# Kernel tuning notes

Hardware: AMD Instinct MI355X
Metric: run time of the kernel (lower is better)

Reference implementation:

```python
import jax, jax.numpy as jnp
import numpy as np

EMBED = 1024
HEADS = 16
HEAD_DIM = EMBED // HEADS


def setup_inputs() -> dict:
    key = jax.random.key(0)
    ks = jax.random.split(key, 10)
    N, S, D = 2, 2048, EMBED
    scale = 1.0 / np.sqrt(D)
    inp = {
        "x": jax.random.normal(ks[0], (N, S, D), dtype=jnp.float32),
        "mask": jax.random.randint(ks[1], (N, 1, S, S), 0, 2, dtype=jnp.int32),
        "Wq": jax.random.normal(ks[2], (D, D), dtype=jnp.float32) * scale,
        "bq": jnp.zeros((D,), dtype=jnp.float32),
        "Wk": jax.random.normal(ks[3], (D, D), dtype=jnp.float32) * scale,
        "bk": jnp.zeros((D,), dtype=jnp.float32),
        "Wv": jax.random.normal(ks[4], (D, D), dtype=jnp.float32) * scale,
        "bv": jnp.zeros((D,), dtype=jnp.float32),
        "Wo": jax.random.normal(ks[5], (D, D), dtype=jnp.float32) * scale,
        "bo": jnp.zeros((D,), dtype=jnp.float32),
    }
    return inp


def reference(x, mask, Wq, bq, Wk, bk, Wv, bv, Wo, bo):
    N, S, D = x.shape
    H, Hd = HEADS, HEAD_DIM
    def split_heads(t):
        return t.reshape(N, S, H, Hd).transpose(0, 2, 1, 3)  # [N,H,S,Hd]
    q = split_heads(x @ Wq + bq)
    k = split_heads(x @ Wk + bk)
    v = split_heads(x @ Wv + bv)
    scores = jnp.einsum("nhqd,nhkd->nhqk", q, k) / jnp.sqrt(jnp.float32(Hd))
    scores = jnp.where(mask == 0, jnp.float32(-jnp.inf), scores)
    attn = jax.nn.softmax(scores, axis=-1)
    out = jnp.einsum("nhqk,nhkd->nhqd", attn, v)
    out = out.transpose(0, 2, 1, 3).reshape(N, S, D)
    return out @ Wo + bo
```

## Files before the change

### kernel.cpp

```cpp
#include <hip/hip_runtime.h>
#include <stdint.h>


typedef _Float16 h8 __attribute__((ext_vector_type(8)));
typedef _Float16 h4 __attribute__((ext_vector_type(4)));
typedef float f32x4 __attribute__((ext_vector_type(4)));

#define MFMA16(a, b, c) __builtin_amdgcn_mfma_f32_16x16x32_f16(a, b, c, 0, 0, 0)

static __device__ __forceinline__ int swz128(int row, int colB) {
    return (row * 128 + colB) ^ ((row & 7) << 4);
}

__global__ __launch_bounds__(256) void k_pack_mask(const int* __restrict__ mask,
                                                   uint32_t* __restrict__ mp) {
    int i = blockIdx.x * 256 + threadIdx.x;
    unsigned long long b = __ballot(mask[i] != 0);
    if ((threadIdx.x & 63) == 0) {
        *(unsigned long long*)(mp + (i >> 5)) = b;
    }
}

__global__ __launch_bounds__(256) void k_wt(const float* __restrict__ W0,
                                            const float* __restrict__ W1,
                                            const float* __restrict__ W2,
                                            _Float16* __restrict__ out) {
    const int nb = blockIdx.x, kb = blockIdx.y, z = blockIdx.z;
    const float* W = (z == 0) ? W0 : ((z == 1) ? W1 : W2);
    _Float16* O = out + (size_t)z * 1024 * 1024;
    __shared__ __align__(16) _Float16 lds[64][68];
    const int t = threadIdx.x;
    const int k0 = kb * 64, n0 = nb * 64;
#pragma unroll
    for (int p = 0; p < 4; ++p) {
        int idx = t + p * 256;
        int kr = idx >> 4;
        int c = idx & 15;
        float4 v = *(const float4*)(W + (size_t)(k0 + kr) * 1024 + n0 + c * 4);
        h4 hv;
        hv[0] = (_Float16)v.x; hv[1] = (_Float16)v.y;
        hv[2] = (_Float16)v.z; hv[3] = (_Float16)v.w;
        *(h4*)(&lds[kr][c * 4]) = hv;
    }
    __syncthreads();
#pragma unroll
    for (int p = 0; p < 2; ++p) {
        int idx = t + p * 256;
        int n = idx >> 3;
        int kc = idx & 7;
        h8 o;
#pragma unroll
        for (int i = 0; i < 8; ++i) o[i] = lds[kc * 8 + i][n];
        *(h8*)(O + (size_t)(n0 + n) * 1024 + k0 + kc * 8) = o;
    }
}

__global__ __launch_bounds__(256) void k_qkv(const float* __restrict__ X,
                                             const _Float16* __restrict__ Wt,
                                             const float* __restrict__ bq,
                                             const float* __restrict__ bk,
                                             const float* __restrict__ bv,
                                             _Float16* __restrict__ Qo,
                                             _Float16* __restrict__ Ko,
                                             _Float16* __restrict__ VtO) {
    const int nt = blockIdx.x;
    const int mt = blockIdx.y;
    const int z = blockIdx.z;
    const _Float16* W = Wt + (size_t)z * 1024 * 1024;
    const float* bias = (z == 0) ? bq : ((z == 1) ? bk : bv);

    __shared__ __align__(16) char lds[32768];
    char* As = lds;
    char* Bs = lds + 16384;

    const int t = threadIdx.x;
    const int lane = t & 63;
    const int w = t >> 6;
    const int wm = w >> 1, wn = w & 1;
    const int m0 = mt * 128, n0 = nt * 128;

    f32x4 acc[4][4] = {};

    for (int kt = 0; kt < 16; ++kt) {
        const int k0 = kt * 64;
#pragma unroll
        for (int p = 0; p < 8; ++p) {
            int idx = t + p * 256;
            int row = idx >> 4;
            int c4 = idx & 15;
            float4 v = *(const float4*)(X + (size_t)(m0 + row) * 1024 + k0 + c4 * 4);
            h4 hv;
            hv[0] = (_Float16)v.x; hv[1] = (_Float16)v.y;
            hv[2] = (_Float16)v.z; hv[3] = (_Float16)v.w;
            *(h4*)(As + swz128(row, c4 * 8)) = hv;
        }
#pragma unroll
        for (int p = 0; p < 4; ++p) {
            int idx = t + p * 256;
            int row = idx >> 3;
            int c = idx & 7;
            uint4 v = *(const uint4*)(W + (size_t)(n0 + row) * 1024 + k0 + c * 8);
            *(uint4*)(Bs + swz128(row, c * 16)) = v;
        }
        __syncthreads();

#pragma unroll
        for (int kk = 0; kk < 2; ++kk) {
            h8 af[4], bf[4];
#pragma unroll
            for (int fm = 0; fm < 4; ++fm)
                af[fm] = *(h8*)(As + swz128(wm * 64 + fm * 16 + (lane & 15),
                                            kk * 64 + (lane >> 4) * 16));
#pragma unroll
            for (int fn = 0; fn < 4; ++fn)
                bf[fn] = *(h8*)(Bs + swz128(wn * 64 + fn * 16 + (lane & 15),
                                            kk * 64 + (lane >> 4) * 16));
#pragma unroll
            for (int fm = 0; fm < 4; ++fm)
#pragma unroll
                for (int fn = 0; fn < 4; ++fn)
                    acc[fm][fn] = MFMA16(af[fm], bf[fn], acc[fm][fn]);
        }
        __syncthreads();
    }

    if (z == 2) {
#pragma unroll
        for (int fn = 0; fn < 4; ++fn) {
            int n = n0 + wn * 64 + fn * 16 + (lane & 15);
            float bv_ = bias[n];
            int h = n >> 6, d = n & 63;
#pragma unroll
            for (int fm = 0; fm < 4; ++fm) {
                int m_base = m0 + wm * 64 + fm * 16 + (lane >> 4) * 4;
                int bi = m_base >> 11, s0 = m_base & 2047;
                h4 pv;
#pragma unroll
                for (int r = 0; r < 4; ++r) pv[r] = (_Float16)(acc[fm][fn][r] + bv_);
                *(h4*)(VtO + ((size_t)((bi * 16 + h) * 64 + d)) * 2048 + s0) = pv;
            }
        }
    } else {
        _Float16* Out = (z == 0) ? Qo : Ko;
#pragma unroll
        for (int fn = 0; fn < 4; ++fn) {
            int n = n0 + wn * 64 + fn * 16 + (lane & 15);
            float bv_ = bias[n];
            int h = n >> 6, d = n & 63;
#pragma unroll
            for (int fm = 0; fm < 4; ++fm) {
#pragma unroll
                for (int r = 0; r < 4; ++r) {
                    int m = m0 + wm * 64 + fm * 16 + (lane >> 4) * 4 + r;
                    int bi = m >> 11, s = m & 2047;
                    float val = acc[fm][fn][r] + bv_;
                    Out[(size_t)((bi * 16 + h) * 2048 + s) * 64 + d] = (_Float16)val;
                }
            }
        }
    }
}

__global__ __launch_bounds__(256) void k_attn(const _Float16* __restrict__ Q,
                                              const _Float16* __restrict__ K,
                                              const _Float16* __restrict__ Vt,
                                              const uint32_t* __restrict__ mp,
                                              _Float16* __restrict__ ctx) {
    const int qt = blockIdx.x;
    const int nh = blockIdx.y;
    const int bi = nh >> 4;
    const int t = threadIdx.x, lane = t & 63, w = t >> 6;
    const int g = lane >> 4;
    const int q15 = lane & 15;

    __shared__ __align__(16) char lds[24576];
    char* Ks = lds;
    char* Vs = lds + 8192;
    char* Ps = lds + 16384 + w * 2048;

    const int qbase = qt * 64 + w * 16;

    h8 qf[2];
#pragma unroll
    for (int kk = 0; kk < 2; ++kk)
        qf[kk] = *(const h8*)(Q + ((size_t)nh * 2048 + qbase + q15) * 64 + kk * 32 + g * 8);

    f32x4 of[4] = {};
    float lacc = 0.f;

    const size_t kbase = (size_t)nh * 2048 * 64;
    const size_t vbase = (size_t)nh * 64 * 2048;
    const float C1 = 0.18033688f;
    const float C2 = 11.541560f;

    for (int kt = 0; kt < 32; ++kt) {
#pragma unroll
        for (int p = 0; p < 2; ++p) {
            int c = t + p * 256;
            int row = c >> 3;
            int cb = (c & 7) * 16;
            uint4 kv = *(const uint4*)(K + kbase + (size_t)kt * 4096 + c * 8);
            *(uint4*)(Ks + swz128(row, cb)) = kv;
            uint4 vv = *(const uint4*)(Vt + vbase + (size_t)row * 2048 + kt * 64 + (c & 7) * 8);
            *(uint4*)(Vs + swz128(row, cb)) = vv;
        }
        __syncthreads();

        f32x4 sf[4];
#pragma unroll
        for (int fn = 0; fn < 4; ++fn) {
            f32x4 a = {};
#pragma unroll
            for (int kk = 0; kk < 2; ++kk) {
                h8 kf = *(h8*)(Ks + swz128(fn * 16 + q15, kk * 64 + g * 16));
                a = MFMA16(kf, qf[kk], a);
            }
            sf[fn] = a;
        }

        {
            uint2 mw = *(const uint2*)(mp + ((size_t)bi * 2048 + qbase + q15) * 64 + kt * 2);
#pragma unroll
            for (int fn = 0; fn < 4; ++fn) {
                uint32_t word = (fn & 2) ? mw.y : mw.x;
                int bitbase = ((fn & 1) << 4) + g * 4;
                h4 pv4;
#pragma unroll
                for (int r = 0; r < 4; ++r) {
                    float p = ((word >> (bitbase + r)) & 1u)
                                  ? __builtin_amdgcn_exp2f(fmaf(sf[fn][r], C1, -C2))
                                  : 0.f;
                    lacc += p;
                    pv4[r] = (_Float16)p;
                }
                *(h4*)(Ps + swz128(q15, (fn * 16 + g * 4) * 2)) = pv4;
            }
        }

        h8 pa[2];
#pragma unroll
        for (int kk = 0; kk < 2; ++kk)
            pa[kk] = *(h8*)(Ps + swz128(q15, kk * 64 + g * 16));
#pragma unroll
        for (int fn = 0; fn < 4; ++fn) {
#pragma unroll
            for (int kk = 0; kk < 2; ++kk) {
                h8 vb = *(h8*)(Vs + swz128(fn * 16 + q15, kk * 64 + g * 16));
                of[fn] = MFMA16(pa[kk], vb, of[fn]);
            }
        }
        __syncthreads();
    }

    lacc += __shfl_xor(lacc, 16);
    lacc += __shfl_xor(lacc, 32);

#pragma unroll
    for (int r = 0; r < 4; ++r) {
        float lq = __shfl(lacc, g * 4 + r);
        int srow = qbase + g * 4 + r;
#pragma unroll
        for (int fn = 0; fn < 4; ++fn) {
            float val = of[fn][r] / lq;
            ctx[(size_t)(bi * 2048 + srow) * 1024 + (nh & 15) * 64 + fn * 16 + q15] =
                (_Float16)val;
        }
    }
}

__global__ __launch_bounds__(256) void k_oproj(const _Float16* __restrict__ A,
                                               const _Float16* __restrict__ Wot,
                                               const float* __restrict__ bias,
                                               float* __restrict__ out) {
    const int nt = blockIdx.x, mt = blockIdx.y;
    __shared__ __align__(16) char lds[32768];
    char* As = lds;
    char* Bs = lds + 16384;
    const int t = threadIdx.x, lane = t & 63, w = t >> 6;
    const int wm = w >> 1, wn = w & 1;
    const int m0 = mt * 128, n0 = nt * 128;
    f32x4 acc[4][4] = {};

    for (int kt = 0; kt < 16; ++kt) {
        const int k0 = kt * 64;
#pragma unroll
        for (int p = 0; p < 4; ++p) {
            int idx = t + p * 256;
            int row = idx >> 3;
            int c = idx & 7;
            uint4 v = *(const uint4*)(A + (size_t)(m0 + row) * 1024 + k0 + c * 8);
            *(uint4*)(As + swz128(row, c * 16)) = v;
        }
#pragma unroll
        for (int p = 0; p < 4; ++p) {
            int idx = t + p * 256;
            int row = idx >> 3;
            int c = idx & 7;
            uint4 v = *(const uint4*)(Wot + (size_t)(n0 + row) * 1024 + k0 + c * 8);
            *(uint4*)(Bs + swz128(row, c * 16)) = v;
        }
        __syncthreads();

#pragma unroll
        for (int kk = 0; kk < 2; ++kk) {
            h8 af[4], bf[4];
#pragma unroll
            for (int fm = 0; fm < 4; ++fm)
                af[fm] = *(h8*)(As + swz128(wm * 64 + fm * 16 + (lane & 15),
                                            kk * 64 + (lane >> 4) * 16));
#pragma unroll
            for (int fn = 0; fn < 4; ++fn)
                bf[fn] = *(h8*)(Bs + swz128(wn * 64 + fn * 16 + (lane & 15),
                                            kk * 64 + (lane >> 4) * 16));
#pragma unroll
            for (int fm = 0; fm < 4; ++fm)
#pragma unroll
                for (int fn = 0; fn < 4; ++fn)
                    acc[fm][fn] = MFMA16(af[fm], bf[fn], acc[fm][fn]);
        }
        __syncthreads();
    }

#pragma unroll
    for (int fn = 0; fn < 4; ++fn) {
        int n = n0 + wn * 64 + fn * 16 + (lane & 15);
        float b = bias[n];
#pragma unroll
        for (int fm = 0; fm < 4; ++fm) {
#pragma unroll
            for (int r = 0; r < 4; ++r) {
                int m = m0 + wm * 64 + fm * 16 + (lane >> 4) * 4 + r;
                out[(size_t)m * 1024 + n] = acc[fm][fn][r] + b;
            }
        }
    }
}

extern "C" void kernel_launch(void* const* d_in, const int* in_sizes, int n_in,
                              void* d_out, int out_size, void* d_ws, size_t ws_size,
                              hipStream_t stream) {
    const float* x = (const float*)d_in[0];
    const int* mask = (const int*)d_in[1];
    const float* Wq = (const float*)d_in[2];
    const float* bq = (const float*)d_in[3];
    const float* Wk = (const float*)d_in[4];
    const float* bk = (const float*)d_in[5];
    const float* Wv = (const float*)d_in[6];
    const float* bv = (const float*)d_in[7];
    const float* Wo = (const float*)d_in[8];
    const float* bo = (const float*)d_in[9];
    float* out = (float*)d_out;

    char* ws = (char*)d_ws;
    _Float16* Wt = (_Float16*)(ws);
    _Float16* ctx = (_Float16*)(ws);
    _Float16* Q = (_Float16*)(ws + (8u << 20));
    _Float16* Kb = (_Float16*)(ws + (16u << 20));
    _Float16* Vt = (_Float16*)(ws + (24u << 20));
    _Float16* Wot = (_Float16*)(ws + (24u << 20));
    uint32_t* mp = (uint32_t*)(ws + (32u << 20));

    k_pack_mask<<<(2 * 2048 * 2048) / 256, 256, 0, stream>>>(mask, mp);
    k_wt<<<dim3(16, 16, 3), 256, 0, stream>>>(Wq, Wk, Wv, Wt);
    k_qkv<<<dim3(8, 32, 3), 256, 0, stream>>>(x, Wt, bq, bk, bv, Q, Kb, Vt);
    k_attn<<<dim3(32, 32), 256, 0, stream>>>(Q, Kb, Vt, mp, ctx);
    k_wt<<<dim3(16, 16, 1), 256, 0, stream>>>(Wo, Wo, Wo, Wot);
    k_oproj<<<dim3(8, 32), 256, 0, stream>>>(ctx, Wot, bo, out);
}
```

Before: 291.6 us.

## Pre-convert X to fp16 and stage V-transpose stores through LDS

Adds a kernel that converts X to fp16 once, so the QKV GEMM reads half-size fp16 tiles with 16-byte loads instead of converting fp32 tiles again in every N-tile block. The V output transpose now goes through shared memory with a 256-byte swizzle, so the global writes are coalesced 16-byte rows instead of scattered 8-byte stores. The fp16 path runs only when the workspace is large enough, which costs one extra launch and an extra read and write of X.

```diff
diff --git a/kernel.cpp b/kernel.cpp
--- a/kernel.cpp
+++ b/kernel.cpp
@@ -10,6 +10,9 @@
 
 static __device__ __forceinline__ int swz128(int row, int colB) {
     return (row * 128 + colB) ^ ((row & 7) << 4);
+}
+static __device__ __forceinline__ int swz256(int row, int colB) {
+    return (row * 256 + colB) ^ ((row & 15) << 4);
 }
 
 __global__ __launch_bounds__(256) void k_pack_mask(const int* __restrict__ mask,
@@ -19,6 +22,17 @@
     if ((threadIdx.x & 63) == 0) {
         *(unsigned long long*)(mp + (i >> 5)) = b;
     }
+}
+
+__global__ __launch_bounds__(256) void k_xh(const float* __restrict__ X,
+                                            _Float16* __restrict__ Xh) {
+    int i = (blockIdx.x * 256 + threadIdx.x) * 8;
+    float4 a = *(const float4*)(X + i);
+    float4 b = *(const float4*)(X + i + 4);
+    h8 o;
+    o[0] = (_Float16)a.x; o[1] = (_Float16)a.y; o[2] = (_Float16)a.z; o[3] = (_Float16)a.w;
+    o[4] = (_Float16)b.x; o[5] = (_Float16)b.y; o[6] = (_Float16)b.z; o[7] = (_Float16)b.w;
+    *(h8*)(Xh + i) = o;
 }
 
 __global__ __launch_bounds__(256) void k_wt(const float* __restrict__ W0,
@@ -55,7 +69,9 @@
     }
 }
 
-__global__ __launch_bounds__(256) void k_qkv(const float* __restrict__ X,
+__global__ __launch_bounds__(256) void k_qkv(const _Float16* __restrict__ Xh,
+                                             const float* __restrict__ Xf,
+                                             const int use_xh,
                                              const _Float16* __restrict__ Wt,
                                              const float* __restrict__ bq,
                                              const float* __restrict__ bk,
@@ -83,16 +99,27 @@
 
     for (int kt = 0; kt < 16; ++kt) {
         const int k0 = kt * 64;
-#pragma unroll
-        for (int p = 0; p < 8; ++p) {
-            int idx = t + p * 256;
-            int row = idx >> 4;
-            int c4 = idx & 15;
-            float4 v = *(const float4*)(X + (size_t)(m0 + row) * 1024 + k0 + c4 * 4);
-            h4 hv;
-            hv[0] = (_Float16)v.x; hv[1] = (_Float16)v.y;
-            hv[2] = (_Float16)v.z; hv[3] = (_Float16)v.w;
-            *(h4*)(As + swz128(row, c4 * 8)) = hv;
+        if (use_xh) {
+#pragma unroll
+            for (int p = 0; p < 4; ++p) {
+                int idx = t + p * 256;
+                int row = idx >> 3;
+                int c = idx & 7;
+                uint4 v = *(const uint4*)(Xh + (size_t)(m0 + row) * 1024 + k0 + c * 8);
+                *(uint4*)(As + swz128(row, c * 16)) = v;
+            }
+        } else {
+#pragma unroll
+            for (int p = 0; p < 8; ++p) {
+                int idx = t + p * 256;
+                int row = idx >> 4;
+                int c4 = idx & 15;
+                float4 v = *(const float4*)(Xf + (size_t)(m0 + row) * 1024 + k0 + c4 * 4);
+                h4 hv;
+                hv[0] = (_Float16)v.x; hv[1] = (_Float16)v.y;
+                hv[2] = (_Float16)v.z; hv[3] = (_Float16)v.w;
+                *(h4*)(As + swz128(row, c4 * 8)) = hv;
+            }
         }
 #pragma unroll
         for (int p = 0; p < 4; ++p) {
@@ -125,20 +152,30 @@
     }
 
     if (z == 2) {
+        const int bi = m0 >> 11, s0 = m0 & 2047;
 #pragma unroll
         for (int fn = 0; fn < 4; ++fn) {
-            int n = n0 + wn * 64 + fn * 16 + (lane & 15);
-            float bv_ = bias[n];
-            int h = n >> 6, d = n & 63;
+            int n_local = wn * 64 + fn * 16 + (lane & 15);
+            float bv_ = bias[n0 + n_local];
 #pragma unroll
             for (int fm = 0; fm < 4; ++fm) {
-                int m_base = m0 + wm * 64 + fm * 16 + (lane >> 4) * 4;
-                int bi = m_base >> 11, s0 = m_base & 2047;
+                int m_base = wm * 64 + fm * 16 + (lane >> 4) * 4;
                 h4 pv;
 #pragma unroll
                 for (int r = 0; r < 4; ++r) pv[r] = (_Float16)(acc[fm][fn][r] + bv_);
-                *(h4*)(VtO + ((size_t)((bi * 16 + h) * 64 + d)) * 2048 + s0) = pv;
-            }
+                *(h4*)(lds + swz256(n_local, m_base * 2)) = pv;
+            }
+        }
+        __syncthreads();
+#pragma unroll
+        for (int p = 0; p < 8; ++p) {
+            int idx = t + p * 256;
+            int row = idx >> 4;
+            int c16 = idx & 15;
+            uint4 v = *(uint4*)(lds + swz256(row, c16 * 16));
+            int hg = (n0 >> 6) + (row >> 6);
+            int d = row & 63;
+            *(uint4*)(VtO + ((size_t)((bi * 16 + hg) * 64 + d)) * 2048 + s0 + c16 * 8) = v;
         }
     } else {
         _Float16* Out = (z == 0) ? Qo : Ko;
@@ -359,10 +396,15 @@
     _Float16* Vt = (_Float16*)(ws + (24u << 20));
     _Float16* Wot = (_Float16*)(ws + (24u << 20));
     uint32_t* mp = (uint32_t*)(ws + (32u << 20));
+    _Float16* Xh = (_Float16*)(ws + (33u << 20));
+    const int use_xh = (ws_size >= (41u << 20)) ? 1 : 0;
 
     k_pack_mask<<<(2 * 2048 * 2048) / 256, 256, 0, stream>>>(mask, mp);
     k_wt<<<dim3(16, 16, 3), 256, 0, stream>>>(Wq, Wk, Wv, Wt);
-    k_qkv<<<dim3(8, 32, 3), 256, 0, stream>>>(x, Wt, bq, bk, bv, Q, Kb, Vt);
+    if (use_xh) {
+        k_xh<<<(2 * 2048 * 1024) / (256 * 8), 256, 0, stream>>>(x, Xh);
+    }
+    k_qkv<<<dim3(8, 32, 3), 256, 0, stream>>>(Xh, x, use_xh, Wt, bq, bk, bv, Q, Kb, Vt);
     k_attn<<<dim3(32, 32), 256, 0, stream>>>(Q, Kb, Vt, mp, ctx);
     k_wt<<<dim3(16, 16, 1), 256, 0, stream>>>(Wo, Wo, Wo, Wot);
     k_oproj<<<dim3(8, 32), 256, 0, stream>>>(ctx, Wot, bo, out);
```

New measurement: 279.6 us. 4.1% less time.
